# Optimization experiments

Hardware: AMD Instinct MI355X
Metric: run time of the kernel (lower is better)

Reference implementation:

```python
import jax, jax.numpy as jnp
import numpy as np

N_NODES = 100000
N_EDGES = 3200000
IN_DIM = 21
HID = 64


def gcn_conv(x, W, b, src, dst, n):
    # GCNConv: out = D^{-1/2} (A + I) D^{-1/2} (x W) + b
    h = x @ W  # [n, out]
    loop = jnp.arange(n)
    src_all = jnp.concatenate([src, loop])
    dst_all = jnp.concatenate([dst, loop])
    deg = jax.ops.segment_sum(jnp.ones(src_all.shape[0], h.dtype), dst_all,
                              num_segments=n)
    dinv = jax.lax.rsqrt(jnp.maximum(deg, 1.0))  # deg >= 1 with self-loops
    norm = dinv[src_all] * dinv[dst_all]  # [E+n]
    out = jax.ops.segment_sum(h[src_all] * norm[:, None], dst_all,
                              num_segments=n)
    return out + b


def setup_inputs() -> dict:
    key = jax.random.key(0)
    ks = jax.random.split(key, 12)
    def lin(k, fan_in, fan_out):
        bound = 1.0 / np.sqrt(fan_in)
        kw, kb = jax.random.split(k)
        W = jax.random.uniform(kw, (fan_in, fan_out), jnp.float32, -bound, bound)
        b = jax.random.uniform(kb, (fan_out,), jnp.float32, -bound, bound)
        return W, b
    x = jax.random.normal(ks[0], (N_NODES, IN_DIM), jnp.float32)
    edge_index = jax.random.randint(ks[1], (2, N_EDGES), 0, N_NODES, jnp.int64)
    W1, b1 = lin(ks[2], IN_DIM, HID)
    W2, b2 = lin(ks[3], HID, 2 * HID)
    W3, b3 = lin(ks[4], 2 * HID, HID)
    Wl1, bl1 = lin(ks[5], HID, 20)
    Wl2, bl2 = lin(ks[6], 20, 1)
    return {"x": x, "edge_index": edge_index,
            "W1": W1, "b1": b1, "W2": W2, "b2": b2, "W3": W3, "b3": b3,
            "Wl1": Wl1, "bl1": bl1, "Wl2": Wl2, "bl2": bl2}


def reference(x, edge_index, W1, b1, W2, b2, W3, b3, Wl1, bl1, Wl2, bl2):
    n = x.shape[0]
    src, dst = edge_index[0], edge_index[1]
    h = jax.nn.relu(gcn_conv(x, W1, b1, src, dst, n))
    h = jax.nn.relu(gcn_conv(h, W2, b2, src, dst, n))
    h = jax.nn.relu(gcn_conv(h, W3, b3, src, dst, n))
    h = jax.nn.relu(h @ Wl1 + bl1)
    return h @ Wl2 + bl2  # [n, 1]
```

## Files before the change

kernel.cpp:

```cpp
#include <hip/hip_runtime.h>

#define DEV static __device__ __forceinline__

typedef __attribute__((ext_vector_type(8))) short short8;
typedef __attribute__((ext_vector_type(4))) float f32x4;

DEV float bf2f(unsigned short u){ union{unsigned i; float f;} a; a.i=((unsigned)u)<<16; return a.f; }
DEV unsigned short f2bf(float f){ union{unsigned i; float f;} a; a.f=f; unsigned r=a.i+0x7fffu+((a.i>>16)&1u); return (unsigned short)(r>>16); }
DEV float2 bfu2f2(unsigned v){ union{unsigned i; float f;} lo,hi; lo.i=v<<16; hi.i=v&0xffff0000u; return make_float2(lo.f,hi.f); }

#define CB_SHIFT 9
#define CB_NODES 512
#define PK_SHIFT 23
#define PK_MASK  0x7fffffu
#define CHUNK 4096

__global__ __launch_bounds__(256) void coarsehist_kernel(const int* __restrict__ dst,
    int* __restrict__ bcnt, int E, int NB){
  __shared__ int h[256];
  int t=threadIdx.x;
  h[t]=0; __syncthreads();
  int i=blockIdx.x*256+t, st=gridDim.x*256;
  for(;i<E;i+=st) atomicAdd(&h[dst[i]>>CB_SHIFT],1);
  __syncthreads();
  if(t<NB && h[t]) atomicAdd(&bcnt[t],h[t]);
}

__global__ __launch_bounds__(256) void binscan_kernel(const int* __restrict__ bcnt,
    int* __restrict__ binoffs, int* __restrict__ bincur, int NB, int E){
  __shared__ int s[256];
  int t=threadIdx.x;
  int v=(t<NB)?bcnt[t]:0;
  s[t]=v; __syncthreads();
  for(int o=1;o<256;o<<=1){
    int u=(t>=o)?s[t-o]:0;
    __syncthreads();
    if(t>=o) s[t]+=u;
    __syncthreads();
  }
  int ex=s[t]-v;
  if(t<NB){ binoffs[t]=ex; bincur[t]=ex; }
  if(t==0) binoffs[NB]=E;
}

__global__ __launch_bounds__(256) void chunkscatter_kernel(const int* __restrict__ src,
    const int* __restrict__ dst, int* __restrict__ bincur, unsigned* __restrict__ tmp,
    int E, int NB){
  __shared__ int lcnt[256];
  __shared__ int lstart[256];
  __shared__ int lbase[256];
  __shared__ unsigned pk[CHUNK];
  __shared__ int gaddr[CHUNK];
  int t=threadIdx.x;
  lcnt[t]=0; __syncthreads();
  int e0=blockIdx.x*CHUNK, e1=min(e0+CHUNK,E);
  int n=e1-e0;
  unsigned pkr[16]; int binr[16]; int rnk[16];
  #pragma unroll
  for(int q=0;q<16;q++){
    int i=e0+t+q*256;
    if(i<e1){
      int d=dst[i];
      int b=d>>CB_SHIFT;
      binr[q]=b;
      pkr[q]=(unsigned)src[i]|((unsigned)(d&(CB_NODES-1))<<PK_SHIFT);
      rnk[q]=atomicAdd(&lcnt[b],1);
    }
  }
  __syncthreads();
  int c=lcnt[t];
  lstart[t]=c; __syncthreads();
  for(int o=1;o<256;o<<=1){
    int u=(t>=o)?lstart[t-o]:0;
    __syncthreads();
    if(t>=o) lstart[t]+=u;
    __syncthreads();
  }
  int ex=lstart[t]-c;
  __syncthreads();
  lstart[t]=ex;
  lbase[t]=(t<NB&&c)?atomicAdd(&bincur[t],c):0;
  __syncthreads();
  #pragma unroll
  for(int q=0;q<16;q++){
    int i=e0+t+q*256;
    if(i<e1){
      int b=binr[q];
      int p=lstart[b]+rnk[q];
      pk[p]=pkr[q];
      gaddr[p]=lbase[b]+rnk[q];
    }
  }
  __syncthreads();
  for(int p=t;p<n;p+=256) tmp[gaddr[p]]=pk[p];
}

__global__ __launch_bounds__(256) void binsort_kernel(const unsigned* __restrict__ tmp,
    const int* __restrict__ binoffs, int* __restrict__ offs, int* __restrict__ deg,
    float* __restrict__ dinv, int* __restrict__ col, int M){
  __shared__ int cnt[CB_NODES];
  __shared__ int cur[CB_NODES];
  __shared__ int ssum[256];
  int b=blockIdx.x, t=threadIdx.x;
  int n0=b*CB_NODES;
  int e0=binoffs[b], e1=binoffs[b+1];
  cnt[2*t]=0; cnt[2*t+1]=0;
  __syncthreads();
  for(int i=e0+t;i<e1;i+=256) atomicAdd(&cnt[tmp[i]>>PK_SHIFT],1);
  __syncthreads();
  int a=cnt[2*t], c=cnt[2*t+1];
  ssum[t]=a+c; __syncthreads();
  for(int o=1;o<256;o<<=1){
    int u=(t>=o)?ssum[t-o]:0;
    __syncthreads();
    if(t>=o) ssum[t]+=u;
    __syncthreads();
  }
  int ex=e0+ssum[t]-(a+c);
  cur[2*t]=ex; cur[2*t+1]=ex+a;
  int na=n0+2*t, nb=n0+2*t+1;
  if(na<M){ offs[na]=ex;   deg[na]=a; dinv[na]=rsqrtf((float)(a+1)); }
  if(nb<M){ offs[nb]=ex+a; deg[nb]=c; dinv[nb]=rsqrtf((float)(c+1)); }
  __syncthreads();
  for(int i=e0+t;i<e1;i+=256){
    unsigned p=tmp[i];
    int pos=atomicAdd(&cur[p>>PK_SHIFT],1);
    col[pos]=(int)(p&PK_MASK);
  }
}

__global__ __launch_bounds__(256) void scale_kernel(const float* __restrict__ x, const float* __restrict__ dinv,
    uint2* __restrict__ xs, int M){
  int idx=blockIdx.x*256+threadIdx.x;
  if(idx>=M*8) return;
  int n=idx>>3, l=idx&7;
  float dv=dinv[n];
  const float* xr=x+(size_t)n*21;
  int c=4*l;
  float f0=(c  <21)?xr[c  ]*dv:0.f;
  float f1=(c+1<21)?xr[c+1]*dv:0.f;
  float f2v=(c+2<21)?xr[c+2]*dv:0.f;
  float f3=(c+3<21)?xr[c+3]*dv:0.f;
  uint2 v;
  v.x=(unsigned)f2bf(f0)|((unsigned)f2bf(f1)<<16);
  v.y=(unsigned)f2bf(f2v)|((unsigned)f2bf(f3)<<16);
  xs[(size_t)n*8+l]=v;
}

template<int GROUP,bool BR,bool OUTBF>
DEV void agg_body(const uint2* __restrict__ xs, const int* __restrict__ col,
    const int* __restrict__ offs, const int* __restrict__ deg, const float* __restrict__ dinv,
    const float* __restrict__ bias, void* __restrict__ out, int M){
  int gid=blockIdx.x*256+threadIdx.x;
  int node=gid/GROUP, lane=gid%GROUP;
  if(node>=M) return;
  float a0,a1,a2,a3;
  {
    uint2 v=xs[(size_t)node*GROUP+lane];
    float2 p=bfu2f2(v.x), q=bfu2f2(v.y);
    a0=p.x; a1=p.y; a2=q.x; a3=q.y;
  }
  int e0=offs[node], d=deg[node];
  int i=0;
  for(;i+8<=d;i+=8){
    int s[8]; uint2 w[8];
    #pragma unroll
    for(int q=0;q<8;q++) s[q]=col[e0+i+q];
    #pragma unroll
    for(int q=0;q<8;q++) w[q]=xs[(size_t)s[q]*GROUP+lane];
    #pragma unroll
    for(int q=0;q<8;q++){
      float2 p=bfu2f2(w[q].x); a0+=p.x; a1+=p.y;
      p=bfu2f2(w[q].y); a2+=p.x; a3+=p.y;
    }
  }
  for(;i+4<=d;i+=4){
    int s[4]; uint2 w[4];
    #pragma unroll
    for(int q=0;q<4;q++) s[q]=col[e0+i+q];
    #pragma unroll
    for(int q=0;q<4;q++) w[q]=xs[(size_t)s[q]*GROUP+lane];
    #pragma unroll
    for(int q=0;q<4;q++){
      float2 p=bfu2f2(w[q].x); a0+=p.x; a1+=p.y;
      p=bfu2f2(w[q].y); a2+=p.x; a3+=p.y;
    }
  }
  for(;i<d;i++){
    uint2 w=xs[(size_t)col[e0+i]*GROUP+lane];
    float2 p=bfu2f2(w.x); a0+=p.x; a1+=p.y;
    p=bfu2f2(w.y); a2+=p.x; a3+=p.y;
  }
  float dv=dinv[node];
  a0*=dv; a1*=dv; a2*=dv; a3*=dv;
  if constexpr(BR){
    a0=fmaxf(a0+bias[4*lane  ],0.f);
    a1=fmaxf(a1+bias[4*lane+1],0.f);
    a2=fmaxf(a2+bias[4*lane+2],0.f);
    a3=fmaxf(a3+bias[4*lane+3],0.f);
  }
  if constexpr(OUTBF){
    uint2 v;
    v.x=(unsigned)f2bf(a0)|((unsigned)f2bf(a1)<<16);
    v.y=(unsigned)f2bf(a2)|((unsigned)f2bf(a3)<<16);
    ((uint2*)out)[(size_t)node*GROUP+lane]=v;
  } else {
    ((float4*)out)[(size_t)node*GROUP+lane]=make_float4(a0,a1,a2,a3);
  }
}

__global__ __launch_bounds__(256) void agg1_kernel(const uint2* xs, const int* col, const int* offs,
    const int* deg, const float* dinv, uint2* out, int M){
  agg_body<8,false,true>(xs,col,offs,deg,dinv,nullptr,out,M);
}
__global__ __launch_bounds__(256) void agg2_kernel(const uint2* xs, const int* col, const int* offs,
    const int* deg, const float* dinv, uint2* out, int M){
  agg_body<16,false,true>(xs,col,offs,deg,dinv,nullptr,out,M);
}
__global__ __launch_bounds__(256) void agg3_kernel(const uint2* xs, const int* col, const int* offs,
    const int* deg, const float* dinv, const float* bias, float4* out, int M){
  agg_body<16,true,false>(xs,col,offs,deg,dinv,bias,out,M);
}

__global__ __launch_bounds__(256) void wprep_kernel(const float* __restrict__ W,
    unsigned short* __restrict__ Warr, int KS, int RK, int N, int KN){
  int idx=blockIdx.x*256+threadIdx.x;
  if(idx>=KN) return;
  int j=idx&7, l=(idx>>3)&63, t=idx>>9;
  int ks=t%KS, nt=t/KS;
  int k=ks*32+((l>>4)<<3)+j;
  int c=nt*16+(l&15);
  float w=(k<RK)?W[(size_t)k*N+c]:0.f;
  unsigned short hi=f2bf(w);
  unsigned short lo=f2bf(w-bf2f(hi));
  Warr[idx]=hi;
  Warr[KN+idx]=lo;
}

template<int K,int NT,bool BR,bool DV>
DEV void mfma_gemm_body(const unsigned short* __restrict__ X, const unsigned short* __restrict__ Warr,
    const float* __restrict__ bias, const float* __restrict__ dinv, unsigned short* __restrict__ Out, int M){
  constexpr int KS=K/32;
  constexpr int N=NT*16;
  constexpr int KN=K*N;
  int tid=threadIdx.x;
  int lane=tid&63, wave=tid>>6;
  int rowbase=blockIdx.x*64+wave*16;
  int r=rowbase+(lane&15);
  int rc=min(r,M-1);
  const short* Xr=(const short*)(X+(size_t)rc*K+((lane>>4)<<3));
  short8 af[KS];
  #pragma unroll
  for(int ks=0;ks<KS;ks++) af[ks]=*(const short8*)(Xr+ks*32);
  const short* wp=(const short*)Warr+lane*8;
  int colv=lane&15;
  #pragma unroll
  for(int nt=0;nt<NT;nt++){
    f32x4 acc={0.f,0.f,0.f,0.f};
    const short* wnt=wp+nt*KS*512;
    #pragma unroll
    for(int ks=0;ks<KS;ks++){
      short8 bh=*(const short8*)(wnt+ks*512);
      short8 bl=*(const short8*)(wnt+KN+ks*512);
      acc=__builtin_amdgcn_mfma_f32_16x16x32_bf16(af[ks],bh,acc,0,0,0);
      acc=__builtin_amdgcn_mfma_f32_16x16x32_bf16(af[ks],bl,acc,0,0,0);
    }
    int c=nt*16+colv;
    float bv=0.f;
    if constexpr(BR) bv=bias[c];
    #pragma unroll
    for(int reg=0;reg<4;reg++){
      int row=rowbase+((lane>>4)<<2)+reg;
      if(row<M){
        float v=acc[reg];
        if constexpr(BR) v=fmaxf(v+bv,0.f);
        if constexpr(DV) v*=dinv[row];
        Out[(size_t)row*N+c]=f2bf(v);
      }
    }
  }
}

__global__ __launch_bounds__(256) void gemm1m_kernel(const unsigned short* X, const unsigned short* Warr,
    const float* bias, const float* dinv, unsigned short* Out, int M){
  mfma_gemm_body<32,4,true,true>(X,Warr,bias,dinv,Out,M);
}
__global__ __launch_bounds__(256) void gemm2m_kernel(const unsigned short* X, const unsigned short* Warr,
    const float* bias, unsigned short* Out, int M){
  mfma_gemm_body<64,8,true,false>(X,Warr,bias,nullptr,Out,M);
}
__global__ __launch_bounds__(256) void gemm3m_kernel(const unsigned short* X, const unsigned short* Warr,
    const float* dinv, unsigned short* Out, int M){
  mfma_gemm_body<128,4,false,true>(X,Warr,nullptr,dinv,Out,M);
}

__global__ __launch_bounds__(256) void mlp_kernel(const float* __restrict__ h, const float* __restrict__ W1,
    const float* __restrict__ b1, const float* __restrict__ W2, const float* __restrict__ b2,
    float* __restrict__ out, int M){
  __shared__ float W1s[64*20];
  __shared__ float b1s[20];
  __shared__ float W2s[20];
  __shared__ float b2s;
  int tid=threadIdx.x;
  for(int i=tid;i<1280;i+=256) W1s[i]=W1[i];
  if(tid<20){ b1s[tid]=b1[tid]; W2s[tid]=W2[tid]; }
  if(tid==0) b2s=b2[0];
  __syncthreads();
  int n=blockIdx.x*256+tid;
  if(n>=M) return;
  float acc[20];
  #pragma unroll
  for(int j=0;j<20;j++) acc[j]=b1s[j];
  const float4* hp=(const float4*)(h+(size_t)n*64);
  for(int k4=0;k4<16;k4++){
    float4 hv=hp[k4];
    #pragma unroll
    for(int j=0;j<20;j++){
      acc[j]=fmaf(hv.x,W1s[(k4*4+0)*20+j],acc[j]);
      acc[j]=fmaf(hv.y,W1s[(k4*4+1)*20+j],acc[j]);
      acc[j]=fmaf(hv.z,W1s[(k4*4+2)*20+j],acc[j]);
      acc[j]=fmaf(hv.w,W1s[(k4*4+3)*20+j],acc[j]);
    }
  }
  float r=b2s;
  #pragma unroll
  for(int j=0;j<20;j++) r+=fmaxf(acc[j],0.f)*W2s[j];
  out[n]=r;
}

extern "C" void kernel_launch(void* const* d_in, const int* in_sizes, int n_in,
                              void* d_out, int out_size, void* d_ws, size_t ws_size,
                              hipStream_t stream){
  const float* x  =(const float*)d_in[0];
  const int*   ei =(const int*)  d_in[1];
  const float* W1 =(const float*)d_in[2];
  const float* b1 =(const float*)d_in[3];
  const float* W2 =(const float*)d_in[4];
  const float* b2 =(const float*)d_in[5];
  const float* W3 =(const float*)d_in[6];
  const float* b3 =(const float*)d_in[7];
  const float* Wl1=(const float*)d_in[8];
  const float* bl1=(const float*)d_in[9];
  const float* Wl2=(const float*)d_in[10];
  const float* bl2=(const float*)d_in[11];
  const int M=in_sizes[0]/21;
  const int E=in_sizes[1]/2;
  const int* srcp=ei;
  const int* dstp=ei+(size_t)E;
  const int NB=(M+CB_NODES-1)/CB_NODES;

  char* ws=(char*)d_ws;
  size_t off=0;
  auto alloc=[&](size_t bytes)->void*{
    off=(off+255)&~(size_t)255;
    void* p=ws+off; off+=bytes; return p;
  };
  int*   offs   =(int*)  alloc((size_t)M*4);
  int*   deg    =(int*)  alloc((size_t)M*4);
  float* dinv   =(float*)alloc((size_t)M*4);
  int*   bcnt   =(int*)  alloc(256*4);
  int*   binoffs=(int*)  alloc(257*4);
  int*   bincur =(int*)  alloc(256*4);
  unsigned short* W1arr=(unsigned short*)alloc(2*32*64*2);
  unsigned short* W2arr=(unsigned short*)alloc(2*64*128*2);
  unsigned short* W3arr=(unsigned short*)alloc(2*128*64*2);
  int*   col    =(int*)  alloc((size_t)E*4);
  float* A=(float*)alloc((size_t)M*256);
  float* B=(float*)alloc((size_t)M*256);
  float* C=(float*)alloc((size_t)M*256);
  float* D=(float*)alloc((size_t)M*256);
  unsigned* tmp=(unsigned*)A;
  (void)ws_size;(void)n_in;(void)out_size;

  hipMemsetAsync(bcnt,0,256*4,stream);
  coarsehist_kernel<<<512,256,0,stream>>>(dstp,bcnt,E,NB);
  binscan_kernel<<<1,256,0,stream>>>(bcnt,binoffs,bincur,NB,E);
  chunkscatter_kernel<<<(E+CHUNK-1)/CHUNK,256,0,stream>>>(srcp,dstp,bincur,tmp,E,NB);
  binsort_kernel<<<NB,256,0,stream>>>(tmp,binoffs,offs,deg,dinv,col,M);
  wprep_kernel<<<(32*64+255)/256,256,0,stream>>>(W1,W1arr,1,21,64,32*64);
  wprep_kernel<<<(64*128+255)/256,256,0,stream>>>(W2,W2arr,2,64,128,64*128);
  wprep_kernel<<<(128*64+255)/256,256,0,stream>>>(W3,W3arr,4,128,64,128*64);

  scale_kernel<<<(M*8+255)/256,256,0,stream>>>(x,dinv,(uint2*)A,M);
  agg1_kernel<<<(M*8+255)/256,256,0,stream>>>((const uint2*)A,col,offs,deg,dinv,(uint2*)B,M);
  gemm1m_kernel<<<(M+63)/64,256,0,stream>>>((const unsigned short*)B,W1arr,b1,dinv,(unsigned short*)C,M);
  agg2_kernel<<<(M*16+255)/256,256,0,stream>>>((const uint2*)C,col,offs,deg,dinv,(uint2*)D,M);
  gemm2m_kernel<<<(M+63)/64,256,0,stream>>>((const unsigned short*)D,W2arr,b2,(unsigned short*)A,M);
  gemm3m_kernel<<<(M+63)/64,256,0,stream>>>((const unsigned short*)A,W3arr,dinv,(unsigned short*)B,M);
  agg3_kernel<<<(M*16+255)/256,256,0,stream>>>((const uint2*)B,col,offs,deg,dinv,b3,(float4*)C,M);
  mlp_kernel<<<(M+255)/256,256,0,stream>>>(C,Wl1,bl1,Wl2,bl2,(float*)d_out,M);
}
```

Before: 308.4 us.

## Partition CSR neighbors by source window and aggregate windows in phases

The bin sort now sub-sorts each node's neighbor list into four source-index windows and records per-window offsets. Each aggregation thread group handles eight nodes and walks all groups' edges window by window. The aim is that gathers across the GPU concentrate on one quarter of the feature table at a time, so the gather working set fits better in cache. In exchange each group does more serial work, there are fewer concurrent waves, shared memory in the bin sort grows, and extra offset arrays must be stored and read.

```diff
diff --git a/kernel.cpp b/kernel.cpp
--- a/kernel.cpp
+++ b/kernel.cpp
@@ -14,6 +14,7 @@
 #define PK_SHIFT 23
 #define PK_MASK  0x7fffffu
 #define CHUNK 4096
+#define P_WIN 4
 
 __global__ __launch_bounds__(256) void coarsehist_kernel(const int* __restrict__ dst,
     int* __restrict__ bcnt, int E, int NB){
@@ -97,35 +98,53 @@
 
 __global__ __launch_bounds__(256) void binsort_kernel(const unsigned* __restrict__ tmp,
     const int* __restrict__ binoffs, int* __restrict__ offs, int* __restrict__ deg,
-    float* __restrict__ dinv, int* __restrict__ col, int M){
-  __shared__ int cnt[CB_NODES];
-  __shared__ int cur[CB_NODES];
+    float* __restrict__ dinv, int* __restrict__ woffs, int* __restrict__ col, int M, int WSZ){
+  __shared__ int cnt[CB_NODES*P_WIN];
+  __shared__ int cur[CB_NODES*P_WIN];
   __shared__ int ssum[256];
   int b=blockIdx.x, t=threadIdx.x;
   int n0=b*CB_NODES;
   int e0=binoffs[b], e1=binoffs[b+1];
-  cnt[2*t]=0; cnt[2*t+1]=0;
-  __syncthreads();
-  for(int i=e0+t;i<e1;i+=256) atomicAdd(&cnt[tmp[i]>>PK_SHIFT],1);
-  __syncthreads();
-  int a=cnt[2*t], c=cnt[2*t+1];
-  ssum[t]=a+c; __syncthreads();
+  for(int i=t;i<CB_NODES*P_WIN;i+=256) cnt[i]=0;
+  __syncthreads();
+  for(int i=e0+t;i<e1;i+=256){
+    unsigned p=tmp[i];
+    int s=(int)(p&PK_MASK);
+    int w=(s>=WSZ)+(s>=2*WSZ)+(s>=3*WSZ);
+    atomicAdd(&cnt[(int)(p>>PK_SHIFT)*P_WIN+w],1);
+  }
+  __syncthreads();
+  int loc[8]; int s=0;
+  #pragma unroll
+  for(int q=0;q<8;q++){ loc[q]=s; s+=cnt[t*8+q]; }
+  ssum[t]=s; __syncthreads();
   for(int o=1;o<256;o<<=1){
     int u=(t>=o)?ssum[t-o]:0;
     __syncthreads();
     if(t>=o) ssum[t]+=u;
     __syncthreads();
   }
-  int ex=e0+ssum[t]-(a+c);
-  cur[2*t]=ex; cur[2*t+1]=ex+a;
-  int na=n0+2*t, nb=n0+2*t+1;
-  if(na<M){ offs[na]=ex;   deg[na]=a; dinv[na]=rsqrtf((float)(a+1)); }
-  if(nb<M){ offs[nb]=ex+a; deg[nb]=c; dinv[nb]=rsqrtf((float)(c+1)); }
+  int base=e0+ssum[t]-s;
+  #pragma unroll
+  for(int q=0;q<8;q++) cur[t*8+q]=base+loc[q];
+  __syncthreads();
+  #pragma unroll
+  for(int h=0;h<2;h++){
+    int nl=2*t+h; int nn=n0+nl;
+    if(nn<M){
+      int dsum=cnt[nl*P_WIN]+cnt[nl*P_WIN+1]+cnt[nl*P_WIN+2]+cnt[nl*P_WIN+3];
+      offs[nn]=cur[nl*P_WIN]; deg[nn]=dsum; dinv[nn]=rsqrtf((float)(dsum+1));
+      #pragma unroll
+      for(int w=0;w<P_WIN;w++) woffs[nn*P_WIN+w]=cur[nl*P_WIN+w];
+    }
+  }
   __syncthreads();
   for(int i=e0+t;i<e1;i+=256){
     unsigned p=tmp[i];
-    int pos=atomicAdd(&cur[p>>PK_SHIFT],1);
-    col[pos]=(int)(p&PK_MASK);
+    int s2=(int)(p&PK_MASK);
+    int w=(s2>=WSZ)+(s2>=2*WSZ)+(s2>=3*WSZ);
+    int pos=atomicAdd(&cur[(int)(p>>PK_SHIFT)*P_WIN+w],1);
+    col[pos]=s2;
   }
 }
 
@@ -149,77 +168,92 @@
 
 template<int GROUP,bool BR,bool OUTBF>
 DEV void agg_body(const uint2* __restrict__ xs, const int* __restrict__ col,
-    const int* __restrict__ offs, const int* __restrict__ deg, const float* __restrict__ dinv,
-    const float* __restrict__ bias, void* __restrict__ out, int M){
-  int gid=blockIdx.x*256+threadIdx.x;
-  int node=gid/GROUP, lane=gid%GROUP;
-  if(node>=M) return;
-  float a0,a1,a2,a3;
-  {
-    uint2 v=xs[(size_t)node*GROUP+lane];
-    float2 p=bfu2f2(v.x), q=bfu2f2(v.y);
-    a0=p.x; a1=p.y; a2=q.x; a3=q.y;
-  }
-  int e0=offs[node], d=deg[node];
-  int i=0;
-  for(;i+8<=d;i+=8){
-    int s[8]; uint2 w[8];
+    const int* __restrict__ offs, const int* __restrict__ deg, const int* __restrict__ woffs,
+    const float* __restrict__ dinv, const float* __restrict__ bias, void* __restrict__ out, int M){
+  constexpr int GPB=256/GROUP;
+  constexpr int NPG=8;
+  int t=threadIdx.x;
+  int g=t/GROUP, lane=t%GROUP;
+  int nbase=blockIdx.x*(GPB*NPG)+g*NPG;
+  float acc[NPG][4];
+  #pragma unroll
+  for(int ni=0;ni<NPG;ni++){
+    int n=nbase+ni;
+    if(n<M){
+      uint2 v=xs[(size_t)n*GROUP+lane];
+      float2 p=bfu2f2(v.x), q=bfu2f2(v.y);
+      acc[ni][0]=p.x; acc[ni][1]=p.y; acc[ni][2]=q.x; acc[ni][3]=q.y;
+    } else {
+      acc[ni][0]=0.f; acc[ni][1]=0.f; acc[ni][2]=0.f; acc[ni][3]=0.f;
+    }
+  }
+  #pragma unroll
+  for(int p=0;p<P_WIN;p++){
     #pragma unroll
-    for(int q=0;q<8;q++) s[q]=col[e0+i+q];
-    #pragma unroll
-    for(int q=0;q<8;q++) w[q]=xs[(size_t)s[q]*GROUP+lane];
-    #pragma unroll
-    for(int q=0;q<8;q++){
-      float2 p=bfu2f2(w[q].x); a0+=p.x; a1+=p.y;
-      p=bfu2f2(w[q].y); a2+=p.x; a3+=p.y;
-    }
-  }
-  for(;i+4<=d;i+=4){
-    int s[4]; uint2 w[4];
-    #pragma unroll
-    for(int q=0;q<4;q++) s[q]=col[e0+i+q];
-    #pragma unroll
-    for(int q=0;q<4;q++) w[q]=xs[(size_t)s[q]*GROUP+lane];
-    #pragma unroll
-    for(int q=0;q<4;q++){
-      float2 p=bfu2f2(w[q].x); a0+=p.x; a1+=p.y;
-      p=bfu2f2(w[q].y); a2+=p.x; a3+=p.y;
-    }
-  }
-  for(;i<d;i++){
-    uint2 w=xs[(size_t)col[e0+i]*GROUP+lane];
-    float2 p=bfu2f2(w.x); a0+=p.x; a1+=p.y;
-    p=bfu2f2(w.y); a2+=p.x; a3+=p.y;
-  }
-  float dv=dinv[node];
-  a0*=dv; a1*=dv; a2*=dv; a3*=dv;
-  if constexpr(BR){
-    a0=fmaxf(a0+bias[4*lane  ],0.f);
-    a1=fmaxf(a1+bias[4*lane+1],0.f);
-    a2=fmaxf(a2+bias[4*lane+2],0.f);
-    a3=fmaxf(a3+bias[4*lane+3],0.f);
-  }
-  if constexpr(OUTBF){
-    uint2 v;
-    v.x=(unsigned)f2bf(a0)|((unsigned)f2bf(a1)<<16);
-    v.y=(unsigned)f2bf(a2)|((unsigned)f2bf(a3)<<16);
-    ((uint2*)out)[(size_t)node*GROUP+lane]=v;
-  } else {
-    ((float4*)out)[(size_t)node*GROUP+lane]=make_float4(a0,a1,a2,a3);
+    for(int ni=0;ni<NPG;ni++){
+      int n=nbase+ni;
+      if(n>=M) continue;
+      int st=woffs[n*P_WIN+p];
+      int en=(p<P_WIN-1)?woffs[n*P_WIN+p+1]:(offs[n]+deg[n]);
+      int i=st;
+      for(;i+4<=en;i+=4){
+        int s0=col[i],s1=col[i+1],s2=col[i+2],s3=col[i+3];
+        uint2 w0=xs[(size_t)s0*GROUP+lane];
+        uint2 w1=xs[(size_t)s1*GROUP+lane];
+        uint2 w2=xs[(size_t)s2*GROUP+lane];
+        uint2 w3=xs[(size_t)s3*GROUP+lane];
+        float2 q;
+        q=bfu2f2(w0.x); acc[ni][0]+=q.x; acc[ni][1]+=q.y;
+        q=bfu2f2(w0.y); acc[ni][2]+=q.x; acc[ni][3]+=q.y;
+        q=bfu2f2(w1.x); acc[ni][0]+=q.x; acc[ni][1]+=q.y;
+        q=bfu2f2(w1.y); acc[ni][2]+=q.x; acc[ni][3]+=q.y;
+        q=bfu2f2(w2.x); acc[ni][0]+=q.x; acc[ni][1]+=q.y;
+        q=bfu2f2(w2.y); acc[ni][2]+=q.x; acc[ni][3]+=q.y;
+        q=bfu2f2(w3.x); acc[ni][0]+=q.x; acc[ni][1]+=q.y;
+        q=bfu2f2(w3.y); acc[ni][2]+=q.x; acc[ni][3]+=q.y;
+      }
+      for(;i<en;i++){
+        uint2 w=xs[(size_t)col[i]*GROUP+lane];
+        float2 q;
+        q=bfu2f2(w.x); acc[ni][0]+=q.x; acc[ni][1]+=q.y;
+        q=bfu2f2(w.y); acc[ni][2]+=q.x; acc[ni][3]+=q.y;
+      }
+    }
+  }
+  #pragma unroll
+  for(int ni=0;ni<NPG;ni++){
+    int n=nbase+ni;
+    if(n>=M) continue;
+    float dv=dinv[n];
+    float a0=acc[ni][0]*dv, a1=acc[ni][1]*dv, a2=acc[ni][2]*dv, a3=acc[ni][3]*dv;
+    if constexpr(BR){
+      a0=fmaxf(a0+bias[4*lane  ],0.f);
+      a1=fmaxf(a1+bias[4*lane+1],0.f);
+      a2=fmaxf(a2+bias[4*lane+2],0.f);
+      a3=fmaxf(a3+bias[4*lane+3],0.f);
+    }
+    if constexpr(OUTBF){
+      uint2 v;
+      v.x=(unsigned)f2bf(a0)|((unsigned)f2bf(a1)<<16);
+      v.y=(unsigned)f2bf(a2)|((unsigned)f2bf(a3)<<16);
+      ((uint2*)out)[(size_t)n*GROUP+lane]=v;
+    } else {
+      ((float4*)out)[(size_t)n*GROUP+lane]=make_float4(a0,a1,a2,a3);
+    }
   }
 }
 
 __global__ __launch_bounds__(256) void agg1_kernel(const uint2* xs, const int* col, const int* offs,
-    const int* deg, const float* dinv, uint2* out, int M){
-  agg_body<8,false,true>(xs,col,offs,deg,dinv,nullptr,out,M);
+    const int* deg, const int* woffs, const float* dinv, uint2* out, int M){
+  agg_body<8,false,true>(xs,col,offs,deg,woffs,dinv,nullptr,out,M);
 }
 __global__ __launch_bounds__(256) void agg2_kernel(const uint2* xs, const int* col, const int* offs,
-    const int* deg, const float* dinv, uint2* out, int M){
-  agg_body<16,false,true>(xs,col,offs,deg,dinv,nullptr,out,M);
+    const int* deg, const int* woffs, const float* dinv, uint2* out, int M){
+  agg_body<16,false,true>(xs,col,offs,deg,woffs,dinv,nullptr,out,M);
 }
 __global__ __launch_bounds__(256) void agg3_kernel(const uint2* xs, const int* col, const int* offs,
-    const int* deg, const float* dinv, const float* bias, float4* out, int M){
-  agg_body<16,true,false>(xs,col,offs,deg,dinv,bias,out,M);
+    const int* deg, const int* woffs, const float* dinv, const float* bias, float4* out, int M){
+  agg_body<16,true,false>(xs,col,offs,deg,woffs,dinv,bias,out,M);
 }
 
 __global__ __launch_bounds__(256) void wprep_kernel(const float* __restrict__ W,
@@ -348,6 +382,7 @@
   const int* srcp=ei;
   const int* dstp=ei+(size_t)E;
   const int NB=(M+CB_NODES-1)/CB_NODES;
+  const int WSZ=(M+P_WIN-1)/P_WIN;
 
   char* ws=(char*)d_ws;
   size_t off=0;
@@ -358,6 +393,7 @@
   int*   offs   =(int*)  alloc((size_t)M*4);
   int*   deg    =(int*)  alloc((size_t)M*4);
   float* dinv   =(float*)alloc((size_t)M*4);
+  int*   woffs  =(int*)  alloc((size_t)M*4*P_WIN);
   int*   bcnt   =(int*)  alloc(256*4);
   int*   binoffs=(int*)  alloc(257*4);
   int*   bincur =(int*)  alloc(256*4);
@@ -376,17 +412,17 @@
   coarsehist_kernel<<<512,256,0,stream>>>(dstp,bcnt,E,NB);
   binscan_kernel<<<1,256,0,stream>>>(bcnt,binoffs,bincur,NB,E);
   chunkscatter_kernel<<<(E+CHUNK-1)/CHUNK,256,0,stream>>>(srcp,dstp,bincur,tmp,E,NB);
-  binsort_kernel<<<NB,256,0,stream>>>(tmp,binoffs,offs,deg,dinv,col,M);
+  binsort_kernel<<<NB,256,0,stream>>>(tmp,binoffs,offs,deg,dinv,woffs,col,M,WSZ);
   wprep_kernel<<<(32*64+255)/256,256,0,stream>>>(W1,W1arr,1,21,64,32*64);
   wprep_kernel<<<(64*128+255)/256,256,0,stream>>>(W2,W2arr,2,64,128,64*128);
   wprep_kernel<<<(128*64+255)/256,256,0,stream>>>(W3,W3arr,4,128,64,128*64);
 
   scale_kernel<<<(M*8+255)/256,256,0,stream>>>(x,dinv,(uint2*)A,M);
-  agg1_kernel<<<(M*8+255)/256,256,0,stream>>>((const uint2*)A,col,offs,deg,dinv,(uint2*)B,M);
+  agg1_kernel<<<(M+255)/256,256,0,stream>>>((const uint2*)A,col,offs,deg,woffs,dinv,(uint2*)B,M);
   gemm1m_kernel<<<(M+63)/64,256,0,stream>>>((const unsigned short*)B,W1arr,b1,dinv,(unsigned short*)C,M);
-  agg2_kernel<<<(M*16+255)/256,256,0,stream>>>((const uint2*)C,col,offs,deg,dinv,(uint2*)D,M);
+  agg2_kernel<<<(M+127)/128,256,0,stream>>>((const uint2*)C,col,offs,deg,woffs,dinv,(uint2*)D,M);
   gemm2m_kernel<<<(M+63)/64,256,0,stream>>>((const unsigned short*)D,W2arr,b2,(unsigned short*)A,M);
   gemm3m_kernel<<<(M+63)/64,256,0,stream>>>((const unsigned short*)A,W3arr,dinv,(unsigned short*)B,M);
-  agg3_kernel<<<(M*16+255)/256,256,0,stream>>>((const uint2*)B,col,offs,deg,dinv,b3,(float4*)C,M);
+  agg3_kernel<<<(M+127)/128,256,0,stream>>>((const uint2*)B,col,offs,deg,woffs,dinv,b3,(float4*)C,M);
   mlp_kernel<<<(M+255)/256,256,0,stream>>>(C,Wl1,bl1,Wl2,bl2,(float*)d_out,M);
 }
```

After: 968.3 us. 214% more time.
